# Kernel optimization log

Hardware: AMD Instinct MI355X
Metric: run time of the kernel (lower is better)

Reference implementation:

```python
import jax, jax.numpy as jnp
import numpy as np

N = 100000   # nodes
E = 1600000  # edges
G = 64       # graphs in batch
IN, H, F1, OUT = 3, 64, 256, 10
EPS = 1e-5


def setup_inputs() -> dict:
    key = jax.random.key(0)
    ks = jax.random.split(key, 16)
    d = {}
    d["x"] = jax.random.normal(ks[0], (N, IN), dtype=jnp.float32)
    d["membership"] = jnp.sort(jax.random.randint(ks[1], (N,), 0, G))
    d["edges"] = jax.random.randint(ks[2], (2, E), 0, N)
    def lin(k, fan_in, shape):
        return jax.random.uniform(k, shape, jnp.float32, -1.0, 1.0) / np.sqrt(fan_in)
    # GraphConv1: out = lin_rel(agg) + lin_root(x); lin_root has no bias in PyG
    d["W_rel1"] = lin(ks[3], IN, (IN, H)); d["b_rel1"] = jnp.zeros((H,), jnp.float32)
    d["W_root1"] = lin(ks[4], IN, (IN, H))
    d["W_rel2"] = lin(ks[5], H, (H, H)); d["b_rel2"] = jnp.zeros((H,), jnp.float32)
    d["W_root2"] = lin(ks[6], H, (H, H))
    d["g1"] = jnp.ones((H,), jnp.float32); d["b1"] = jnp.zeros((H,), jnp.float32)
    d["g2"] = jnp.ones((H,), jnp.float32); d["b2"] = jnp.zeros((H,), jnp.float32)
    d["W_fc1"] = lin(ks[7], H, (H, F1)); d["b_fc1"] = lin(ks[8], H, (F1,))
    d["g3"] = jnp.ones((F1,), jnp.float32); d["b3"] = jnp.zeros((F1,), jnp.float32)
    d["W_fc2"] = lin(ks[9], F1, (F1, OUT)); d["b_fc2"] = lin(ks[10], F1, (OUT,))
    return d


def _bn(h, g, b):
    # BatchNorm1d in training mode: biased batch variance
    m = h.mean(axis=0)
    v = h.var(axis=0)
    return (h - m) * jax.lax.rsqrt(v + EPS) * g + b


def reference(x, membership, edges, W_rel1, b_rel1, W_root1, W_rel2, b_rel2,
              W_root2, g1, b1, g2, b2, W_fc1, b_fc1, g3, b3, W_fc2, b_fc2):
    src, dst = edges[0], edges[1]

    def gconv(h, Wr, br, Wroot):
        # message = x_j (edge_weight=None); aggr='add' at target node
        agg = jax.ops.segment_sum(h[src], dst, num_segments=N)
        return agg @ Wr + br + h @ Wroot

    h = _bn(jax.nn.relu(gconv(x, W_rel1, b_rel1, W_root1)), g1, b1)
    h = _bn(jax.nn.relu(gconv(h, W_rel2, b_rel2, W_root2)), g2, b2)
    # global mean pool over graph membership
    cnt = jax.ops.segment_sum(jnp.ones((N,), h.dtype), membership, num_segments=G)
    pooled = jax.ops.segment_sum(h, membership, num_segments=G) / jnp.maximum(cnt, 1.0)[:, None]
    z = _bn(jax.nn.relu(pooled @ W_fc1 + b_fc1), g3, b3)
    return z @ W_fc2 + b_fc2
```

## Files before the change

kernel.cpp:

```cpp
#include <hip/hip_runtime.h>
#include <hip/hip_bf16.h>

#define EPSV 1e-5f
#define BKT 128
#define NB  782

typedef __hip_bfloat16 bf16;
typedef __attribute__((ext_vector_type(8))) short short8v;
typedef __attribute__((ext_vector_type(4))) float f32x4v;

__device__ inline void atomAddG(float* p, float v) { unsafeAtomicAdd(p, v); }
__device__ inline unsigned short f2bf(float v) {
    bf16 h = __float2bfloat16(v);
    return *reinterpret_cast<unsigned short*>(&h);
}

__global__ __launch_bounds__(256) void bhist_kernel(
    const int* __restrict__ edges, int* __restrict__ gbcnt, int E)
{
    __shared__ int lh[NB];
    const int t = threadIdx.x;
    for (int i = t; i < NB; i += 256) lh[i] = 0;
    __syncthreads();
    const int base = blockIdx.x * 4096;
    #pragma unroll
    for (int i = 0; i < 16; ++i) {
        int e = base + i * 256 + t;
        if (e < E) atomicAdd(&lh[edges[E + e] >> 7], 1);
    }
    __syncthreads();
    for (int i = t; i < NB; i += 256) {
        int c = lh[i];
        if (c) atomicAdd(&gbcnt[i], c);
    }
}

__global__ __launch_bounds__(256) void bscan_kernel(
    const int* __restrict__ gbcnt, int* __restrict__ bbase,
    int* __restrict__ gcursor, int E)
{
    __shared__ int l[256];
    const int t = threadIdx.x;
    int b0 = t * 4;
    int v0 = (b0 + 0 < NB) ? gbcnt[b0 + 0] : 0;
    int v1 = (b0 + 1 < NB) ? gbcnt[b0 + 1] : 0;
    int v2 = (b0 + 2 < NB) ? gbcnt[b0 + 2] : 0;
    int v3 = (b0 + 3 < NB) ? gbcnt[b0 + 3] : 0;
    int tot = v0 + v1 + v2 + v3;
    l[t] = tot;
    __syncthreads();
    for (int o = 1; o < 256; o <<= 1) {
        int add = (t >= o) ? l[t - o] : 0;
        __syncthreads();
        l[t] += add;
        __syncthreads();
    }
    int off = l[t] - tot;
    if (b0 + 0 < NB) { bbase[b0 + 0] = off;                gcursor[b0 + 0] = off; }
    if (b0 + 1 < NB) { bbase[b0 + 1] = off + v0;           gcursor[b0 + 1] = off + v0; }
    if (b0 + 2 < NB) { bbase[b0 + 2] = off + v0 + v1;      gcursor[b0 + 2] = off + v0 + v1; }
    if (b0 + 3 < NB) { bbase[b0 + 3] = off + v0 + v1 + v2; gcursor[b0 + 3] = off + v0 + v1 + v2; }
    if (t == 0) bbase[NB] = E;
}

__global__ __launch_bounds__(256) void bfill_kernel(
    const int* __restrict__ edges, int* __restrict__ gcursor,
    int* __restrict__ pk, int E)
{
    __shared__ int lh[NB];
    __shared__ int lbase[NB];
    const int t = threadIdx.x;
    for (int i = t; i < NB; i += 256) lh[i] = 0;
    __syncthreads();
    const int base = blockIdx.x * 4096;
    int dv[16];
    #pragma unroll
    for (int i = 0; i < 16; ++i) {
        int e = base + i * 256 + t;
        dv[i] = (e < E) ? edges[E + e] : -1;
        if (dv[i] >= 0) atomicAdd(&lh[dv[i] >> 7], 1);
    }
    __syncthreads();
    for (int i = t; i < NB; i += 256) {
        int c = lh[i];
        lbase[i] = c ? atomicAdd(&gcursor[i], c) : 0;
        lh[i] = 0;
    }
    __syncthreads();
    #pragma unroll
    for (int i = 0; i < 16; ++i) {
        int e = base + i * 256 + t;
        if (dv[i] >= 0) {
            int s = edges[e];
            int b = dv[i] >> 7;
            int pos = lbase[b] + atomicAdd(&lh[b], 1);
            pk[pos] = (s << 7) | (dv[i] & 127);
        }
    }
}

__global__ __launch_bounds__(256) void bsort_kernel(
    const int* __restrict__ pk, const int* __restrict__ bbase,
    const float* __restrict__ x,
    int* __restrict__ rowstart, int* __restrict__ srcs,
    float* __restrict__ agg1, int N, int E)
{
    __shared__ int lcnt[BKT];
    __shared__ int lscan[BKT];
    __shared__ float accx[BKT * 4];
    const int t = threadIdx.x;
    const int b = blockIdx.x;
    const int e0 = bbase[b], e1 = bbase[b + 1];
    if (t < BKT) lcnt[t] = 0;
    for (int i = t; i < BKT * 4; i += 256) accx[i] = 0.f;
    __syncthreads();
    for (int e = e0 + t; e < e1; e += 256) atomicAdd(&lcnt[pk[e] & 127], 1);
    __syncthreads();
    if (t < BKT) lscan[t] = lcnt[t];
    __syncthreads();
    for (int o = 1; o < BKT; o <<= 1) {
        int add = (t < BKT && t >= o) ? lscan[t - o] : 0;
        __syncthreads();
        if (t < BKT) lscan[t] += add;
        __syncthreads();
    }
    const int n0 = b * BKT;
    if (t < BKT) {
        int excl = lscan[t] - lcnt[t];
        lscan[t] = excl;
        int n = n0 + t;
        if (n <= N) rowstart[n] = e0 + excl;
        lcnt[t] = 0;
    }
    __syncthreads();
    for (int e = e0 + t; e < e1; e += 256) {
        int v = pk[e];
        int ld = v & 127;
        int s = v >> 7;
        int pos = atomicAdd(&lcnt[ld], 1);
        srcs[e0 + lscan[ld] + pos] = s;
        atomicAdd(&accx[ld * 4 + 0], x[s * 3 + 0]);
        atomicAdd(&accx[ld * 4 + 1], x[s * 3 + 1]);
        atomicAdd(&accx[ld * 4 + 2], x[s * 3 + 2]);
    }
    __syncthreads();
    for (int i = t; i < BKT * 3; i += 256) {
        int nl = i / 3, c = i - nl * 3;
        int n = n0 + nl;
        if (n < N) agg1[n * 3 + c] = accx[nl * 4 + c];
    }
}

__global__ __launch_bounds__(256) void bounds_kernel(
    const int* __restrict__ membership, int* __restrict__ gstart, int N)
{
    int n = blockIdx.x * 256 + threadIdx.x;
    if (n > N) return;
    int mp = (n == 0) ? -1 : membership[n - 1];
    int mc = (n == N) ? 64 : membership[n];
    for (int g = mp + 1; g <= mc; ++g) gstart[g] = n;
}

__global__ __launch_bounds__(256) void layer1_kernel(
    const float* __restrict__ x, const float* __restrict__ agg1,
    const float* __restrict__ W_rel1, const float* __restrict__ b_rel1,
    const float* __restrict__ W_root1,
    unsigned short* __restrict__ u1b, float* __restrict__ sums, float* __restrict__ sumsq,
    int N)
{
    const int t = threadIdx.x;
    const int f = t & 63, r4 = t >> 6;
    const float wr0 = W_rel1[f], wr1 = W_rel1[64 + f], wr2 = W_rel1[128 + f];
    const float wo0 = W_root1[f], wo1 = W_root1[64 + f], wo2 = W_root1[128 + f];
    const float bb = b_rel1[f];
    float ps = 0.f, pq = 0.f;
    const int base = blockIdx.x * 128;
    for (int i = r4; i < 128; i += 4) {
        int n = base + i;
        if (n >= N) break;
        float a0 = agg1[n * 3 + 0], a1 = agg1[n * 3 + 1], a2 = agg1[n * 3 + 2];
        float x0 = x[n * 3 + 0], x1 = x[n * 3 + 1], x2 = x[n * 3 + 2];
        float v = bb;
        v = fmaf(a0, wr0, v); v = fmaf(a1, wr1, v); v = fmaf(a2, wr2, v);
        v = fmaf(x0, wo0, v); v = fmaf(x1, wo1, v); v = fmaf(x2, wo2, v);
        v = fmaxf(v, 0.f);
        u1b[n * 64 + f] = f2bf(v);
        ps += v; pq += v * v;
    }
    __shared__ float lsum[4][64], lsq[4][64];
    lsum[r4][f] = ps; lsq[r4][f] = pq;
    __syncthreads();
    if (r4 == 0) {
        float s = lsum[0][f] + lsum[1][f] + lsum[2][f] + lsum[3][f];
        float q = lsq[0][f] + lsq[1][f] + lsq[2][f] + lsq[3][f];
        atomAddG(&sums[f], s);
        atomAddG(&sumsq[f], q);
    }
}

__global__ void bnscale_kernel(const float* __restrict__ sums, const float* __restrict__ sumsq,
                               const float* __restrict__ g, const float* __restrict__ b,
                               float invn, int C,
                               float* __restrict__ scale, float* __restrict__ shift)
{
    int f = blockIdx.x * blockDim.x + threadIdx.x;
    if (f >= C) return;
    float m = sums[f] * invn;
    float v = sumsq[f] * invn - m * m;
    float sc = g[f] * rsqrtf(v + EPSV);
    scale[f] = sc;
    shift[f] = b[f] - m * sc;
}

__global__ __launch_bounds__(256) void bnfold_kernel(
    const float* __restrict__ scale1, const float* __restrict__ shift1,
    const float* __restrict__ W_rel2, const float* __restrict__ W_root2,
    const float* __restrict__ b_rel2,
    unsigned short* __restrict__ wrelp, unsigned short* __restrict__ wrootp,
    float* __restrict__ crel, float* __restrict__ croot)
{
    __shared__ float r1[4][64], r2[4][64];
    const int t = threadIdx.x, f = t & 63, kg = t >> 6;
    float c1 = 0.f, c2 = 0.f;
    for (int k = kg * 16; k < kg * 16 + 16; ++k) {
        float sc = scale1[k], sh = shift1[k];
        float w1 = W_rel2[k * 64 + f], w2 = W_root2[k * 64 + f];
        wrelp[k * 64 + f] = f2bf(sc * w1);
        wrootp[k * 64 + f] = f2bf(sc * w2);
        c1 = fmaf(sh, w1, c1); c2 = fmaf(sh, w2, c2);
    }
    r1[kg][f] = c1; r2[kg][f] = c2;
    __syncthreads();
    if (kg == 0) {
        crel[f]  = r1[0][f] + r1[1][f] + r1[2][f] + r1[3][f];
        croot[f] = r2[0][f] + r2[1][f] + r2[2][f] + r2[3][f] + b_rel2[f];
    }
}

__global__ __launch_bounds__(256) void mfma_transform_kernel(
    const unsigned short* __restrict__ u1b,
    const unsigned short* __restrict__ wrelp, const unsigned short* __restrict__ wrootp,
    const float* __restrict__ crel, const float* __restrict__ croot,
    unsigned short* __restrict__ tb, unsigned short* __restrict__ pb, int NT)
{
    const int wid = (blockIdx.x * blockDim.x + threadIdx.x) >> 6;
    const int lane = threadIdx.x & 63;
    const int q = lane >> 4, r = lane & 15;

    short8v Bf[2][8];
    float cadd[8];
    #pragma unroll
    for (int kc = 0; kc < 2; ++kc) {
        #pragma unroll
        for (int ft = 0; ft < 8; ++ft) {
            const unsigned short* W = (ft < 4) ? wrelp : wrootp;
            const int f0 = (ft & 3) * 16;
            short8v b;
            #pragma unroll
            for (int j = 0; j < 8; ++j) {
                int k = 32 * kc + 8 * q + j;
                b[j] = (short)W[k * 64 + f0 + r];
            }
            Bf[kc][ft] = b;
        }
    }
    #pragma unroll
    for (int ft = 0; ft < 8; ++ft)
        cadd[ft] = (ft < 4) ? crel[(ft & 3) * 16 + r] : croot[(ft & 3) * 16 + r];

    const int totalWaves = (gridDim.x * blockDim.x) >> 6;
    for (int tile = wid; tile < NT; tile += totalWaves) {
        const int n0 = tile * 16;
        short8v A0 = *(const short8v*)&u1b[(n0 + r) * 64 + 8 * q];
        short8v A1 = *(const short8v*)&u1b[(n0 + r) * 64 + 32 + 8 * q];
        #pragma unroll
        for (int ft = 0; ft < 8; ++ft) {
            f32x4v d = {0.f, 0.f, 0.f, 0.f};
            d = __builtin_amdgcn_mfma_f32_16x16x32_bf16(A0, Bf[0][ft], d, 0, 0, 0);
            d = __builtin_amdgcn_mfma_f32_16x16x32_bf16(A1, Bf[1][ft], d, 0, 0, 0);
            unsigned short* O = (ft < 4) ? tb : pb;
            const int f0 = (ft & 3) * 16;
            const float ca = cadd[ft];
            #pragma unroll
            for (int rr = 0; rr < 4; ++rr) {
                int n = n0 + 4 * q + rr;
                O[n * 64 + f0 + r] = f2bf(d[rr] + ca);
            }
        }
    }
}

__global__ __launch_bounds__(256, 8) void gatherpool_kernel(
    const bf16* __restrict__ tb, const bf16* __restrict__ pb,
    const int* __restrict__ rowstart, const int* __restrict__ srcs,
    const int* __restrict__ membership,
    float* __restrict__ pooled, float* __restrict__ sums, float* __restrict__ sumsq,
    int N, int chunk)
{
    __shared__ float red[4][64];
    const int tid = threadIdx.x;
    const int w = tid >> 6, f = tid & 63;
    const int gw = __builtin_amdgcn_readfirstlane(blockIdx.x * 4 + w);
    const int n0 = gw * chunk;
    const int n1 = min(N, n0 + chunk);
    float ps = 0.f, pq = 0.f, pacc = 0.f;
    int curg = (n0 < N) ? membership[n0] : -1;

    for (int n = n0; n < n1; ++n) {
        int s0 = rowstart[n], s1 = rowstart[n + 1];
        float acc = __bfloat162float(pb[n * 64 + f]);
        int j = s0;
        for (; j + 15 < s1; j += 16) {
            float vs[16];
            #pragma unroll
            for (int q = 0; q < 16; ++q)
                vs[q] = __bfloat162float(tb[srcs[j + q] * 64 + f]);
            float sA = ((vs[0] + vs[1]) + (vs[2] + vs[3])) + ((vs[4] + vs[5]) + (vs[6] + vs[7]));
            float sB = ((vs[8] + vs[9]) + (vs[10] + vs[11])) + ((vs[12] + vs[13]) + (vs[14] + vs[15]));
            acc += sA + sB;
        }
        for (; j + 3 < s1; j += 4) {
            float v0 = __bfloat162float(tb[srcs[j + 0] * 64 + f]);
            float v1 = __bfloat162float(tb[srcs[j + 1] * 64 + f]);
            float v2 = __bfloat162float(tb[srcs[j + 2] * 64 + f]);
            float v3 = __bfloat162float(tb[srcs[j + 3] * 64 + f]);
            acc += (v0 + v1) + (v2 + v3);
        }
        for (; j < s1; ++j) acc += __bfloat162float(tb[srcs[j] * 64 + f]);

        acc = fmaxf(acc, 0.f);
        ps += acc; pq += acc * acc;

        int g = membership[n];
        if (g != curg) {
            atomAddG(&pooled[curg * 64 + f], pacc);
            pacc = 0.f;
            curg = g;
        }
        pacc += acc;
    }
    if (curg >= 0) atomAddG(&pooled[curg * 64 + f], pacc);

    red[w][f] = ps;
    __syncthreads();
    if (w == 0) atomAddG(&sums[f], red[0][f] + red[1][f] + red[2][f] + red[3][f]);
    __syncthreads();
    red[w][f] = pq;
    __syncthreads();
    if (w == 0) atomAddG(&sumsq[f], red[0][f] + red[1][f] + red[2][f] + red[3][f]);
}

__global__ __launch_bounds__(1024) void fc1_kernel(
    const float* __restrict__ pooled, const int* __restrict__ gstart,
    const float* __restrict__ scale2, const float* __restrict__ shift2,
    const float* __restrict__ W_fc1, const float* __restrict__ b_fc1,
    const float* __restrict__ g3, const float* __restrict__ b3,
    float* __restrict__ z)
{
    __shared__ float pm[4096];
    __shared__ float reds[4][256], redq[4][256];
    __shared__ float lsc[256], lsh[256];
    const int t = threadIdx.x;
    for (int i = t; i < 4096; i += 1024) {
        int g = i >> 6, f = i & 63;
        float c = fmaxf((float)(gstart[g + 1] - gstart[g]), 1.0f);
        pm[i] = fmaf(pooled[i] / c, scale2[f], shift2[f]);
    }
    __syncthreads();
    const int col = t & 255, grp = t >> 8;
    float acc[16];
    const float bc = b_fc1[col];
    #pragma unroll
    for (int g = 0; g < 16; ++g) acc[g] = bc;
    for (int k = 0; k < 64; ++k) {
        float wv = W_fc1[k * 256 + col];
        #pragma unroll
        for (int g = 0; g < 16; ++g)
            acc[g] = fmaf(pm[(grp * 16 + g) * 64 + k], wv, acc[g]);
    }
    float s = 0.f, q = 0.f;
    #pragma unroll
    for (int g = 0; g < 16; ++g) {
        acc[g] = fmaxf(acc[g], 0.f);
        s += acc[g]; q += acc[g] * acc[g];
    }
    reds[grp][col] = s; redq[grp][col] = q;
    __syncthreads();
    if (grp == 0) {
        float S = reds[0][col] + reds[1][col] + reds[2][col] + reds[3][col];
        float Q = redq[0][col] + redq[1][col] + redq[2][col] + redq[3][col];
        float m = S * (1.0f / 64.0f);
        float v = Q * (1.0f / 64.0f) - m * m;
        float sc = g3[col] * rsqrtf(v + EPSV);
        lsc[col] = sc;
        lsh[col] = b3[col] - m * sc;
    }
    __syncthreads();
    float sc = lsc[col], sh = lsh[col];
    #pragma unroll
    for (int g = 0; g < 16; ++g)
        z[(grp * 16 + g) * 256 + col] = fmaf(acc[g], sc, sh);
}

__global__ __launch_bounds__(640) void fc2_kernel(
    const float* __restrict__ z, const float* __restrict__ W_fc2,
    const float* __restrict__ b_fc2, float* __restrict__ out)
{
    int t = threadIdx.x;
    int g = t / 10, o = t % 10;
    float acc = b_fc2[o];
    for (int c = 0; c < 256; ++c)
        acc = fmaf(z[g * 256 + c], W_fc2[c * 10 + o], acc);
    out[g * 10 + o] = acc;
}

extern "C" void kernel_launch(void* const* d_in, const int* in_sizes, int n_in,
                              void* d_out, int out_size, void* d_ws, size_t ws_size,
                              hipStream_t stream) {
    const int N = 100000, E = 1600000;

    const float* x          = (const float*)d_in[0];
    const int*   membership = (const int*)d_in[1];
    const int*   edges      = (const int*)d_in[2];
    const float* W_rel1     = (const float*)d_in[3];
    const float* b_rel1     = (const float*)d_in[4];
    const float* W_root1    = (const float*)d_in[5];
    const float* W_rel2     = (const float*)d_in[6];
    const float* b_rel2     = (const float*)d_in[7];
    const float* W_root2    = (const float*)d_in[8];
    const float* g1         = (const float*)d_in[9];
    const float* b1         = (const float*)d_in[10];
    const float* g2         = (const float*)d_in[11];
    const float* b2         = (const float*)d_in[12];
    const float* W_fc1      = (const float*)d_in[13];
    const float* b_fc1      = (const float*)d_in[14];
    const float* g3         = (const float*)d_in[15];
    const float* b3         = (const float*)d_in[16];
    const float* W_fc2      = (const float*)d_in[17];
    const float* b_fc2      = (const float*)d_in[18];

    int*   wsi      = (int*)d_ws;
    float* wsf      = (float*)d_ws;
    int*   gbcnt    = wsi + 0;
    float* stats    = wsf + 784;
    float* pooled   = wsf + 1296;
    int*   bbase    = wsi + 5392;
    int*   gcursor  = wsi + 6192;
    int*   gstart   = wsi + 6976;
    int*   rowstart = wsi + 7104;
    int*   pk       = wsi + 107168;
    int*   srcs     = wsi + 1707168;
    float* agg1     = wsf + 3307168;
    unsigned short* u1b = (unsigned short*)(wsf + 3607200);
    unsigned short* tb  = (unsigned short*)(wsf + 6807200);
    unsigned short* pb  = (unsigned short*)(wsf + 10007200);
    unsigned short* wrelp  = (unsigned short*)(wsf + 13207200);
    unsigned short* wrootp = (unsigned short*)(wsf + 13209248);
    float* crel     = wsf + 13211296;
    float* croot    = wsf + 13211360;
    float* z        = wsf + 13211424;

    float* sums1  = stats + 0;
    float* sumsq1 = stats + 64;
    float* sums2  = stats + 128;
    float* sumsq2 = stats + 192;
    float* scale1 = stats + 256;
    float* shift1 = stats + 320;
    float* scale2 = stats + 384;
    float* shift2 = stats + 448;

    hipMemsetAsync(d_ws, 0, (size_t)(784 + 512 + 4096) * 4, stream);

    const int EB = (E + 4095) / 4096;
    bhist_kernel<<<EB, 256, 0, stream>>>(edges, gbcnt, E);
    bscan_kernel<<<1, 256, 0, stream>>>(gbcnt, bbase, gcursor, E);
    bfill_kernel<<<EB, 256, 0, stream>>>(edges, gcursor, pk, E);
    bsort_kernel<<<NB, 256, 0, stream>>>(pk, bbase, x, rowstart, srcs, agg1, N, E);
    bounds_kernel<<<(N + 256) / 256, 256, 0, stream>>>(membership, gstart, N);

    layer1_kernel<<<(N + 127) / 128, 256, 0, stream>>>(
        x, agg1, W_rel1, b_rel1, W_root1, u1b, sums1, sumsq1, N);
    bnscale_kernel<<<1, 64, 0, stream>>>(sums1, sumsq1, g1, b1, 1.0f / N, 64, scale1, shift1);

    bnfold_kernel<<<1, 256, 0, stream>>>(scale1, shift1, W_rel2, W_root2, b_rel2,
                                         wrelp, wrootp, crel, croot);
    mfma_transform_kernel<<<512, 256, 0, stream>>>(
        u1b, wrelp, wrootp, crel, croot, tb, pb, N / 16);

    {
        const int GRID2 = 2048;
        int chunk = (N + GRID2 * 4 - 1) / (GRID2 * 4);
        gatherpool_kernel<<<GRID2, 256, 0, stream>>>(
            (const bf16*)tb, (const bf16*)pb, rowstart, srcs, membership,
            pooled, sums2, sumsq2, N, chunk);
    }
    bnscale_kernel<<<1, 64, 0, stream>>>(sums2, sumsq2, g2, b2, 1.0f / N, 64, scale2, shift2);

    fc1_kernel<<<1, 1024, 0, stream>>>(pooled, gstart, scale2, shift2,
                                       W_fc1, b_fc1, g3, b3, z);
    fc2_kernel<<<1, 640, 0, stream>>>(z, W_fc2, b_fc2, (float*)d_out);
}
```

Before: 254.3 us.

## Use 1024-node sort buckets, interleave two-row gathers, fuse BN-scale and fc kernels

The counting sort now uses 98 buckets of 1024 destinations instead of 782 buckets of 128, and the per-bucket sort runs with 1024-thread blocks. The gather-pool loop processes two destination rows at once with 8-wide unrolls, so more independent loads are in flight. The layer-1 BN scale computation is folded into bnfold, and fc2 is merged into fc1, which removes two launches. The trade-off is that the bucket sort kernel gets only 98 blocks, which gives low parallelism on a large GPU.

```diff
diff --git a/kernel.cpp b/kernel.cpp
--- a/kernel.cpp
+++ b/kernel.cpp
@@ -2,8 +2,8 @@
 #include <hip/hip_bf16.h>
 
 #define EPSV 1e-5f
-#define BKT 128
-#define NB  782
+#define CB   1024
+#define NBC  98
 
 typedef __hip_bfloat16 bf16;
 typedef __attribute__((ext_vector_type(8))) short short8v;
@@ -14,63 +14,61 @@
     bf16 h = __float2bfloat16(v);
     return *reinterpret_cast<unsigned short*>(&h);
 }
+__device__ inline float bfu(unsigned short u) {
+    return __uint_as_float(((unsigned int)u) << 16);
+}
 
 __global__ __launch_bounds__(256) void bhist_kernel(
     const int* __restrict__ edges, int* __restrict__ gbcnt, int E)
 {
-    __shared__ int lh[NB];
+    __shared__ int lh[NBC];
     const int t = threadIdx.x;
-    for (int i = t; i < NB; i += 256) lh[i] = 0;
+    if (t < NBC) lh[t] = 0;
     __syncthreads();
     const int base = blockIdx.x * 4096;
     #pragma unroll
     for (int i = 0; i < 16; ++i) {
         int e = base + i * 256 + t;
-        if (e < E) atomicAdd(&lh[edges[E + e] >> 7], 1);
-    }
-    __syncthreads();
-    for (int i = t; i < NB; i += 256) {
-        int c = lh[i];
-        if (c) atomicAdd(&gbcnt[i], c);
-    }
-}
-
-__global__ __launch_bounds__(256) void bscan_kernel(
+        if (e < E) atomicAdd(&lh[edges[E + e] >> 10], 1);
+    }
+    __syncthreads();
+    if (t < NBC) {
+        int c = lh[t];
+        if (c) atomicAdd(&gbcnt[t], c);
+    }
+}
+
+__global__ __launch_bounds__(128) void bscan_kernel(
     const int* __restrict__ gbcnt, int* __restrict__ bbase,
     int* __restrict__ gcursor, int E)
 {
-    __shared__ int l[256];
+    __shared__ int l[128];
     const int t = threadIdx.x;
-    int b0 = t * 4;
-    int v0 = (b0 + 0 < NB) ? gbcnt[b0 + 0] : 0;
-    int v1 = (b0 + 1 < NB) ? gbcnt[b0 + 1] : 0;
-    int v2 = (b0 + 2 < NB) ? gbcnt[b0 + 2] : 0;
-    int v3 = (b0 + 3 < NB) ? gbcnt[b0 + 3] : 0;
-    int tot = v0 + v1 + v2 + v3;
-    l[t] = tot;
-    __syncthreads();
-    for (int o = 1; o < 256; o <<= 1) {
+    int v = (t < NBC) ? gbcnt[t] : 0;
+    l[t] = v;
+    __syncthreads();
+    for (int o = 1; o < 128; o <<= 1) {
         int add = (t >= o) ? l[t - o] : 0;
         __syncthreads();
         l[t] += add;
         __syncthreads();
     }
-    int off = l[t] - tot;
-    if (b0 + 0 < NB) { bbase[b0 + 0] = off;                gcursor[b0 + 0] = off; }
-    if (b0 + 1 < NB) { bbase[b0 + 1] = off + v0;           gcursor[b0 + 1] = off + v0; }
-    if (b0 + 2 < NB) { bbase[b0 + 2] = off + v0 + v1;      gcursor[b0 + 2] = off + v0 + v1; }
-    if (b0 + 3 < NB) { bbase[b0 + 3] = off + v0 + v1 + v2; gcursor[b0 + 3] = off + v0 + v1 + v2; }
-    if (t == 0) bbase[NB] = E;
+    if (t < NBC) {
+        int off = l[t] - v;
+        bbase[t] = off;
+        gcursor[t] = off;
+    }
+    if (t == 0) bbase[NBC] = E;
 }
 
 __global__ __launch_bounds__(256) void bfill_kernel(
     const int* __restrict__ edges, int* __restrict__ gcursor,
     int* __restrict__ pk, int E)
 {
-    __shared__ int lh[NB];
-    __shared__ int lbase[NB];
+    __shared__ int lh[NBC];
+    __shared__ int lbase[NBC];
     const int t = threadIdx.x;
-    for (int i = t; i < NB; i += 256) lh[i] = 0;
+    if (t < NBC) lh[t] = 0;
     __syncthreads();
     const int base = blockIdx.x * 4096;
     int dv[16];
@@ -78,13 +76,13 @@
     for (int i = 0; i < 16; ++i) {
         int e = base + i * 256 + t;
         dv[i] = (e < E) ? edges[E + e] : -1;
-        if (dv[i] >= 0) atomicAdd(&lh[dv[i] >> 7], 1);
-    }
-    __syncthreads();
-    for (int i = t; i < NB; i += 256) {
-        int c = lh[i];
-        lbase[i] = c ? atomicAdd(&gcursor[i], c) : 0;
-        lh[i] = 0;
+        if (dv[i] >= 0) atomicAdd(&lh[dv[i] >> 10], 1);
+    }
+    __syncthreads();
+    if (t < NBC) {
+        int c = lh[t];
+        lbase[t] = c ? atomicAdd(&gcursor[t], c) : 0;
+        lh[t] = 0;
     }
     __syncthreads();
     #pragma unroll
@@ -92,51 +90,50 @@
         int e = base + i * 256 + t;
         if (dv[i] >= 0) {
             int s = edges[e];
-            int b = dv[i] >> 7;
+            int b = dv[i] >> 10;
             int pos = lbase[b] + atomicAdd(&lh[b], 1);
-            pk[pos] = (s << 7) | (dv[i] & 127);
-        }
-    }
-}
-
-__global__ __launch_bounds__(256) void bsort_kernel(
+            pk[pos] = (s << 10) | (dv[i] & 1023);
+        }
+    }
+}
+
+__global__ __launch_bounds__(1024) void bsortB_kernel(
     const int* __restrict__ pk, const int* __restrict__ bbase,
     const float* __restrict__ x,
     int* __restrict__ rowstart, int* __restrict__ srcs,
     float* __restrict__ agg1, int N, int E)
 {
-    __shared__ int lcnt[BKT];
-    __shared__ int lscan[BKT];
-    __shared__ float accx[BKT * 4];
+    __shared__ int lcnt[CB];
+    __shared__ int lscan[CB];
+    __shared__ float accx[CB * 4];
     const int t = threadIdx.x;
     const int b = blockIdx.x;
     const int e0 = bbase[b], e1 = bbase[b + 1];
-    if (t < BKT) lcnt[t] = 0;
-    for (int i = t; i < BKT * 4; i += 256) accx[i] = 0.f;
-    __syncthreads();
-    for (int e = e0 + t; e < e1; e += 256) atomicAdd(&lcnt[pk[e] & 127], 1);
-    __syncthreads();
-    if (t < BKT) lscan[t] = lcnt[t];
-    __syncthreads();
-    for (int o = 1; o < BKT; o <<= 1) {
-        int add = (t < BKT && t >= o) ? lscan[t - o] : 0;
+    lcnt[t] = 0;
+    #pragma unroll
+    for (int i = 0; i < 4; ++i) accx[i * CB + t] = 0.f;
+    __syncthreads();
+    for (int e = e0 + t; e < e1; e += 1024) atomicAdd(&lcnt[pk[e] & 1023], 1);
+    __syncthreads();
+    lscan[t] = lcnt[t];
+    __syncthreads();
+    for (int o = 1; o < CB; o <<= 1) {
+        int add = (t >= o) ? lscan[t - o] : 0;
         __syncthreads();
-        if (t < BKT) lscan[t] += add;
+        lscan[t] += add;
         __syncthreads();
     }
-    const int n0 = b * BKT;
-    if (t < BKT) {
-        int excl = lscan[t] - lcnt[t];
-        lscan[t] = excl;
-        int n = n0 + t;
-        if (n <= N) rowstart[n] = e0 + excl;
-        lcnt[t] = 0;
-    }
-    __syncthreads();
-    for (int e = e0 + t; e < e1; e += 256) {
+    const int n0 = b * CB;
+    int excl = lscan[t] - lcnt[t];
+    int n = n0 + t;
+    if (n <= N) rowstart[n] = e0 + excl;
+    lscan[t] = excl;
+    lcnt[t] = 0;
+    __syncthreads();
+    for (int e = e0 + t; e < e1; e += 1024) {
         int v = pk[e];
-        int ld = v & 127;
-        int s = v >> 7;
+        int ld = v & 1023;
+        int s = v >> 10;
         int pos = atomicAdd(&lcnt[ld], 1);
         srcs[e0 + lscan[ld] + pos] = s;
         atomicAdd(&accx[ld * 4 + 0], x[s * 3 + 0]);
@@ -144,10 +141,10 @@
         atomicAdd(&accx[ld * 4 + 2], x[s * 3 + 2]);
     }
     __syncthreads();
-    for (int i = t; i < BKT * 3; i += 256) {
+    for (int i = t; i < CB * 3; i += 1024) {
         int nl = i / 3, c = i - nl * 3;
-        int n = n0 + nl;
-        if (n < N) agg1[n * 3 + c] = accx[nl * 4 + c];
+        int nn = n0 + nl;
+        if (nn < N) agg1[nn * 3 + c] = accx[nl * 4 + c];
     }
 }
 
@@ -213,17 +210,27 @@
 }
 
 __global__ __launch_bounds__(256) void bnfold_kernel(
-    const float* __restrict__ scale1, const float* __restrict__ shift1,
+    const float* __restrict__ sums1, const float* __restrict__ sumsq1,
+    const float* __restrict__ g1, const float* __restrict__ b1,
     const float* __restrict__ W_rel2, const float* __restrict__ W_root2,
     const float* __restrict__ b_rel2,
     unsigned short* __restrict__ wrelp, unsigned short* __restrict__ wrootp,
-    float* __restrict__ crel, float* __restrict__ croot)
-{
+    float* __restrict__ crel, float* __restrict__ croot, float invn)
+{
+    __shared__ float lsc[64], lsh[64];
     __shared__ float r1[4][64], r2[4][64];
     const int t = threadIdx.x, f = t & 63, kg = t >> 6;
+    if (t < 64) {
+        float m = sums1[t] * invn;
+        float v = sumsq1[t] * invn - m * m;
+        float sc = g1[t] * rsqrtf(v + EPSV);
+        lsc[t] = sc;
+        lsh[t] = b1[t] - m * sc;
+    }
+    __syncthreads();
     float c1 = 0.f, c2 = 0.f;
     for (int k = kg * 16; k < kg * 16 + 16; ++k) {
-        float sc = scale1[k], sh = shift1[k];
+        float sc = lsc[k], sh = lsh[k];
         float w1 = W_rel2[k * 64 + f], w2 = W_root2[k * 64 + f];
         wrelp[k * 64 + f] = f2bf(sc * w1);
         wrootp[k * 64 + f] = f2bf(sc * w2);
@@ -255,13 +262,13 @@
         for (int ft = 0; ft < 8; ++ft) {
             const unsigned short* W = (ft < 4) ? wrelp : wrootp;
             const int f0 = (ft & 3) * 16;
-            short8v b;
+            short8v bb;
             #pragma unroll
             for (int j = 0; j < 8; ++j) {
                 int k = 32 * kc + 8 * q + j;
-                b[j] = (short)W[k * 64 + f0 + r];
+                bb[j] = (short)W[k * 64 + f0 + r];
             }
-            Bf[kc][ft] = b;
+            Bf[kc][ft] = bb;
         }
     }
     #pragma unroll
@@ -291,7 +298,7 @@
 }
 
 __global__ __launch_bounds__(256, 8) void gatherpool_kernel(
-    const bf16* __restrict__ tb, const bf16* __restrict__ pb,
+    const unsigned short* __restrict__ tb, const unsigned short* __restrict__ pb,
     const int* __restrict__ rowstart, const int* __restrict__ srcs,
     const int* __restrict__ membership,
     float* __restrict__ pooled, float* __restrict__ sums, float* __restrict__ sumsq,
@@ -306,38 +313,60 @@
     float ps = 0.f, pq = 0.f, pacc = 0.f;
     int curg = (n0 < N) ? membership[n0] : -1;
 
-    for (int n = n0; n < n1; ++n) {
-        int s0 = rowstart[n], s1 = rowstart[n + 1];
-        float acc = __bfloat162float(pb[n * 64 + f]);
-        int j = s0;
-        for (; j + 15 < s1; j += 16) {
-            float vs[16];
+    for (int n = n0; n < n1; n += 2) {
+        const bool two = (n + 1 < n1);
+        int sA0 = rowstart[n], sA1 = rowstart[n + 1];
+        int sB1 = two ? rowstart[n + 2] : sA1;
+        int degA = sA1 - sA0, degB = sB1 - sA1;
+        float accA = bfu(pb[n * 64 + f]);
+        float accB = two ? bfu(pb[(n + 1) * 64 + f]) : 0.f;
+
+        int mA = degA & ~7, mB = degB & ~7;
+        int m = min(mA, mB);
+        int k = 0;
+        for (; k < m; k += 8) {
+            float va[8], vb[8];
             #pragma unroll
-            for (int q = 0; q < 16; ++q)
-                vs[q] = __bfloat162float(tb[srcs[j + q] * 64 + f]);
-            float sA = ((vs[0] + vs[1]) + (vs[2] + vs[3])) + ((vs[4] + vs[5]) + (vs[6] + vs[7]));
-            float sB = ((vs[8] + vs[9]) + (vs[10] + vs[11])) + ((vs[12] + vs[13]) + (vs[14] + vs[15]));
-            acc += sA + sB;
-        }
-        for (; j + 3 < s1; j += 4) {
-            float v0 = __bfloat162float(tb[srcs[j + 0] * 64 + f]);
-            float v1 = __bfloat162float(tb[srcs[j + 1] * 64 + f]);
-            float v2 = __bfloat162float(tb[srcs[j + 2] * 64 + f]);
-            float v3 = __bfloat162float(tb[srcs[j + 3] * 64 + f]);
-            acc += (v0 + v1) + (v2 + v3);
-        }
-        for (; j < s1; ++j) acc += __bfloat162float(tb[srcs[j] * 64 + f]);
-
-        acc = fmaxf(acc, 0.f);
-        ps += acc; pq += acc * acc;
-
-        int g = membership[n];
-        if (g != curg) {
+            for (int u = 0; u < 8; ++u) va[u] = bfu(tb[srcs[sA0 + k + u] * 64 + f]);
+            #pragma unroll
+            for (int u = 0; u < 8; ++u) vb[u] = bfu(tb[srcs[sA1 + k + u] * 64 + f]);
+            accA += ((va[0] + va[1]) + (va[2] + va[3])) + ((va[4] + va[5]) + (va[6] + va[7]));
+            accB += ((vb[0] + vb[1]) + (vb[2] + vb[3])) + ((vb[4] + vb[5]) + (vb[6] + vb[7]));
+        }
+        for (int ka = k; ka < mA; ka += 8) {
+            float va[8];
+            #pragma unroll
+            for (int u = 0; u < 8; ++u) va[u] = bfu(tb[srcs[sA0 + ka + u] * 64 + f]);
+            accA += ((va[0] + va[1]) + (va[2] + va[3])) + ((va[4] + va[5]) + (va[6] + va[7]));
+        }
+        for (int kb = k; kb < mB; kb += 8) {
+            float vb[8];
+            #pragma unroll
+            for (int u = 0; u < 8; ++u) vb[u] = bfu(tb[srcs[sA1 + kb + u] * 64 + f]);
+            accB += ((vb[0] + vb[1]) + (vb[2] + vb[3])) + ((vb[4] + vb[5]) + (vb[6] + vb[7]));
+        }
+        for (int ka = mA; ka < degA; ++ka) accA += bfu(tb[srcs[sA0 + ka] * 64 + f]);
+        for (int kb = mB; kb < degB; ++kb) accB += bfu(tb[srcs[sA1 + kb] * 64 + f]);
+
+        accA = fmaxf(accA, 0.f);
+        ps += accA; pq += accA * accA;
+        int gA = membership[n];
+        if (gA != curg) {
             atomAddG(&pooled[curg * 64 + f], pacc);
-            pacc = 0.f;
-            curg = g;
-        }
-        pacc += acc;
+            pacc = 0.f; curg = gA;
+        }
+        pacc += accA;
+
+        if (two) {
+            accB = fmaxf(accB, 0.f);
+            ps += accB; pq += accB * accB;
+            int gB = membership[n + 1];
+            if (gB != curg) {
+                atomAddG(&pooled[curg * 64 + f], pacc);
+                pacc = 0.f; curg = gB;
+            }
+            pacc += accB;
+        }
     }
     if (curg >= 0) atomAddG(&pooled[curg * 64 + f], pacc);
 
@@ -350,12 +379,13 @@
     if (w == 0) atomAddG(&sumsq[f], red[0][f] + red[1][f] + red[2][f] + red[3][f]);
 }
 
-__global__ __launch_bounds__(1024) void fc1_kernel(
+__global__ __launch_bounds__(1024) void fc12_kernel(
     const float* __restrict__ pooled, const int* __restrict__ gstart,
     const float* __restrict__ scale2, const float* __restrict__ shift2,
     const float* __restrict__ W_fc1, const float* __restrict__ b_fc1,
     const float* __restrict__ g3, const float* __restrict__ b3,
-    float* __restrict__ z)
+    const float* __restrict__ W_fc2, const float* __restrict__ b_fc2,
+    float* __restrict__ z, float* __restrict__ out)
 {
     __shared__ float pm[4096];
     __shared__ float reds[4][256], redq[4][256];
@@ -400,18 +430,14 @@
     #pragma unroll
     for (int g = 0; g < 16; ++g)
         z[(grp * 16 + g) * 256 + col] = fmaf(acc[g], sc, sh);
-}
-
-__global__ __launch_bounds__(640) void fc2_kernel(
-    const float* __restrict__ z, const float* __restrict__ W_fc2,
-    const float* __restrict__ b_fc2, float* __restrict__ out)
-{
-    int t = threadIdx.x;
-    int g = t / 10, o = t % 10;
-    float acc = b_fc2[o];
-    for (int c = 0; c < 256; ++c)
-        acc = fmaf(z[g * 256 + c], W_fc2[c * 10 + o], acc);
-    out[g * 10 + o] = acc;
+    __syncthreads();
+    if (t < 640) {
+        int g = t / 10, o = t % 10;
+        float a = b_fc2[o];
+        for (int c = 0; c < 256; ++c)
+            a = fmaf(z[g * 256 + c], W_fc2[c * 10 + o], a);
+        out[g * 10 + o] = a;
+    }
 }
 
 extern "C" void kernel_launch(void* const* d_in, const int* in_sizes, int n_in,
@@ -464,8 +490,6 @@
     float* sumsq1 = stats + 64;
     float* sums2  = stats + 128;
     float* sumsq2 = stats + 192;
-    float* scale1 = stats + 256;
-    float* shift1 = stats + 320;
     float* scale2 = stats + 384;
     float* shift2 = stats + 448;
 
@@ -473,17 +497,17 @@
 
     const int EB = (E + 4095) / 4096;
     bhist_kernel<<<EB, 256, 0, stream>>>(edges, gbcnt, E);
-    bscan_kernel<<<1, 256, 0, stream>>>(gbcnt, bbase, gcursor, E);
+    bscan_kernel<<<1, 128, 0, stream>>>(gbcnt, bbase, gcursor, E);
     bfill_kernel<<<EB, 256, 0, stream>>>(edges, gcursor, pk, E);
-    bsort_kernel<<<NB, 256, 0, stream>>>(pk, bbase, x, rowstart, srcs, agg1, N, E);
+    bsortB_kernel<<<NBC, 1024, 0, stream>>>(pk, bbase, x, rowstart, srcs, agg1, N, E);
     bounds_kernel<<<(N + 256) / 256, 256, 0, stream>>>(membership, gstart, N);
 
     layer1_kernel<<<(N + 127) / 128, 256, 0, stream>>>(
         x, agg1, W_rel1, b_rel1, W_root1, u1b, sums1, sumsq1, N);
-    bnscale_kernel<<<1, 64, 0, stream>>>(sums1, sumsq1, g1, b1, 1.0f / N, 64, scale1, shift1);
-
-    bnfold_kernel<<<1, 256, 0, stream>>>(scale1, shift1, W_rel2, W_root2, b_rel2,
-                                         wrelp, wrootp, crel, croot);
+
+    bnfold_kernel<<<1, 256, 0, stream>>>(sums1, sumsq1, g1, b1,
+                                         W_rel2, W_root2, b_rel2,
+                                         wrelp, wrootp, crel, croot, 1.0f / N);
     mfma_transform_kernel<<<512, 256, 0, stream>>>(
         u1b, wrelp, wrootp, crel, croot, tb, pb, N / 16);
 
@@ -491,12 +515,11 @@
         const int GRID2 = 2048;
         int chunk = (N + GRID2 * 4 - 1) / (GRID2 * 4);
         gatherpool_kernel<<<GRID2, 256, 0, stream>>>(
-            (const bf16*)tb, (const bf16*)pb, rowstart, srcs, membership,
-            pooled, sums2, sumsq2, N, chunk);
+            tb, pb, rowstart, srcs, membership, pooled, sums2, sumsq2, N, chunk);
     }
     bnscale_kernel<<<1, 64, 0, stream>>>(sums2, sumsq2, g2, b2, 1.0f / N, 64, scale2, shift2);
 
-    fc1_kernel<<<1, 1024, 0, stream>>>(pooled, gstart, scale2, shift2,
-                                       W_fc1, b_fc1, g3, b3, z);
-    fc2_kernel<<<1, 640, 0, stream>>>(z, W_fc2, b_fc2, (float*)d_out);
-}
+    fc12_kernel<<<1, 1024, 0, stream>>>(pooled, gstart, scale2, shift2,
+                                        W_fc1, b_fc1, g3, b3, W_fc2, b_fc2,
+                                        z, (float*)d_out);
+}
```

Result: slower. 276.3 us (+8.6%).

## Fuse BN scale kernels, stage bucket keys in LDS, dynamic gather scheduling

Applied to the files above, without the earlier changes.

Folds the BatchNorm scale/shift computation into the consumer kernels and fuses fc1 with fc2, removing three small launches. bsort caches each bucket's packed keys in shared memory to avoid re-reading them, and reads a float4-padded copy of x produced by a new pad kernel. gatherpool replaces static per-wave node ranges with an atomic work cursor handing out 5-node chunks, plus an extra 8-wide tail step. This adds one launch, more pooled atomics per chunk, and cursor contention.

```diff
diff --git a/kernel.cpp b/kernel.cpp
--- a/kernel.cpp
+++ b/kernel.cpp
@@ -4,6 +4,8 @@
 #define EPSV 1e-5f
 #define BKT 128
 #define NB  782
+#define LPK 4096
+#define GCHUNK 5
 
 typedef __hip_bfloat16 bf16;
 typedef __attribute__((ext_vector_type(8))) short short8v;
@@ -13,6 +15,9 @@
 __device__ inline unsigned short f2bf(float v) {
     bf16 h = __float2bfloat16(v);
     return *reinterpret_cast<unsigned short*>(&h);
+}
+__device__ inline float bfu(unsigned short u) {
+    return __uint_as_float(((unsigned int)u) << 16);
 }
 
 __global__ __launch_bounds__(256) void bhist_kernel(
@@ -99,22 +104,38 @@
     }
 }
 
+__global__ __launch_bounds__(256) void xpad_kernel(
+    const float* __restrict__ x, float* __restrict__ xp, int N)
+{
+    int n = blockIdx.x * 256 + threadIdx.x;
+    if (n >= N) return;
+    float4 v;
+    v.x = x[n * 3 + 0]; v.y = x[n * 3 + 1]; v.z = x[n * 3 + 2]; v.w = 0.f;
+    *(float4*)&xp[n * 4] = v;
+}
+
 __global__ __launch_bounds__(256) void bsort_kernel(
     const int* __restrict__ pk, const int* __restrict__ bbase,
-    const float* __restrict__ x,
+    const float* __restrict__ xp,
     int* __restrict__ rowstart, int* __restrict__ srcs,
     float* __restrict__ agg1, int N, int E)
 {
     __shared__ int lcnt[BKT];
     __shared__ int lscan[BKT];
     __shared__ float accx[BKT * 4];
+    __shared__ int lpk[LPK];
     const int t = threadIdx.x;
     const int b = blockIdx.x;
     const int e0 = bbase[b], e1 = bbase[b + 1];
+    const int cnt = e1 - e0;
     if (t < BKT) lcnt[t] = 0;
     for (int i = t; i < BKT * 4; i += 256) accx[i] = 0.f;
-    __syncthreads();
-    for (int e = e0 + t; e < e1; e += 256) atomicAdd(&lcnt[pk[e] & 127], 1);
+    for (int i = t; i < cnt && i < LPK; i += 256) lpk[i] = pk[e0 + i];
+    __syncthreads();
+    for (int i = t; i < cnt; i += 256) {
+        int v = (i < LPK) ? lpk[i] : pk[e0 + i];
+        atomicAdd(&lcnt[v & 127], 1);
+    }
     __syncthreads();
     if (t < BKT) lscan[t] = lcnt[t];
     __syncthreads();
@@ -133,15 +154,16 @@
         lcnt[t] = 0;
     }
     __syncthreads();
-    for (int e = e0 + t; e < e1; e += 256) {
-        int v = pk[e];
+    for (int i = t; i < cnt; i += 256) {
+        int v = (i < LPK) ? lpk[i] : pk[e0 + i];
         int ld = v & 127;
         int s = v >> 7;
         int pos = atomicAdd(&lcnt[ld], 1);
         srcs[e0 + lscan[ld] + pos] = s;
-        atomicAdd(&accx[ld * 4 + 0], x[s * 3 + 0]);
-        atomicAdd(&accx[ld * 4 + 1], x[s * 3 + 1]);
-        atomicAdd(&accx[ld * 4 + 2], x[s * 3 + 2]);
+        float4 xv = *(const float4*)&xp[s * 4];
+        atomicAdd(&accx[ld * 4 + 0], xv.x);
+        atomicAdd(&accx[ld * 4 + 1], xv.y);
+        atomicAdd(&accx[ld * 4 + 2], xv.z);
     }
     __syncthreads();
     for (int i = t; i < BKT * 3; i += 256) {
@@ -198,32 +220,28 @@
     }
 }
 
-__global__ void bnscale_kernel(const float* __restrict__ sums, const float* __restrict__ sumsq,
-                               const float* __restrict__ g, const float* __restrict__ b,
-                               float invn, int C,
-                               float* __restrict__ scale, float* __restrict__ shift)
-{
-    int f = blockIdx.x * blockDim.x + threadIdx.x;
-    if (f >= C) return;
-    float m = sums[f] * invn;
-    float v = sumsq[f] * invn - m * m;
-    float sc = g[f] * rsqrtf(v + EPSV);
-    scale[f] = sc;
-    shift[f] = b[f] - m * sc;
-}
-
 __global__ __launch_bounds__(256) void bnfold_kernel(
-    const float* __restrict__ scale1, const float* __restrict__ shift1,
+    const float* __restrict__ sums1, const float* __restrict__ sumsq1,
+    const float* __restrict__ g1, const float* __restrict__ b1,
     const float* __restrict__ W_rel2, const float* __restrict__ W_root2,
     const float* __restrict__ b_rel2,
     unsigned short* __restrict__ wrelp, unsigned short* __restrict__ wrootp,
-    float* __restrict__ crel, float* __restrict__ croot)
-{
+    float* __restrict__ crel, float* __restrict__ croot, float invn)
+{
+    __shared__ float lsc[64], lsh[64];
     __shared__ float r1[4][64], r2[4][64];
     const int t = threadIdx.x, f = t & 63, kg = t >> 6;
+    if (t < 64) {
+        float m = sums1[t] * invn;
+        float v = sumsq1[t] * invn - m * m;
+        float sc = g1[t] * rsqrtf(v + EPSV);
+        lsc[t] = sc;
+        lsh[t] = b1[t] - m * sc;
+    }
+    __syncthreads();
     float c1 = 0.f, c2 = 0.f;
     for (int k = kg * 16; k < kg * 16 + 16; ++k) {
-        float sc = scale1[k], sh = shift1[k];
+        float sc = lsc[k], sh = lsh[k];
         float w1 = W_rel2[k * 64 + f], w2 = W_root2[k * 64 + f];
         wrelp[k * 64 + f] = f2bf(sc * w1);
         wrootp[k * 64 + f] = f2bf(sc * w2);
@@ -255,13 +273,13 @@
         for (int ft = 0; ft < 8; ++ft) {
             const unsigned short* W = (ft < 4) ? wrelp : wrootp;
             const int f0 = (ft & 3) * 16;
-            short8v b;
+            short8v bb;
             #pragma unroll
             for (int j = 0; j < 8; ++j) {
                 int k = 32 * kc + 8 * q + j;
-                b[j] = (short)W[k * 64 + f0 + r];
+                bb[j] = (short)W[k * 64 + f0 + r];
             }
-            Bf[kc][ft] = b;
+            Bf[kc][ft] = bb;
         }
     }
     #pragma unroll
@@ -291,55 +309,72 @@
 }
 
 __global__ __launch_bounds__(256, 8) void gatherpool_kernel(
-    const bf16* __restrict__ tb, const bf16* __restrict__ pb,
+    const unsigned short* __restrict__ tb, const unsigned short* __restrict__ pb,
     const int* __restrict__ rowstart, const int* __restrict__ srcs,
     const int* __restrict__ membership,
+    int* __restrict__ cursor,
     float* __restrict__ pooled, float* __restrict__ sums, float* __restrict__ sumsq,
-    int N, int chunk)
+    int N)
 {
     __shared__ float red[4][64];
     const int tid = threadIdx.x;
     const int w = tid >> 6, f = tid & 63;
-    const int gw = __builtin_amdgcn_readfirstlane(blockIdx.x * 4 + w);
-    const int n0 = gw * chunk;
-    const int n1 = min(N, n0 + chunk);
-    float ps = 0.f, pq = 0.f, pacc = 0.f;
-    int curg = (n0 < N) ? membership[n0] : -1;
-
-    for (int n = n0; n < n1; ++n) {
-        int s0 = rowstart[n], s1 = rowstart[n + 1];
-        float acc = __bfloat162float(pb[n * 64 + f]);
-        int j = s0;
-        for (; j + 15 < s1; j += 16) {
-            float vs[16];
-            #pragma unroll
-            for (int q = 0; q < 16; ++q)
-                vs[q] = __bfloat162float(tb[srcs[j + q] * 64 + f]);
-            float sA = ((vs[0] + vs[1]) + (vs[2] + vs[3])) + ((vs[4] + vs[5]) + (vs[6] + vs[7]));
-            float sB = ((vs[8] + vs[9]) + (vs[10] + vs[11])) + ((vs[12] + vs[13]) + (vs[14] + vs[15]));
-            acc += sA + sB;
+    float ps = 0.f, pq = 0.f;
+
+    for (;;) {
+        int c = 0;
+        if (f == 0) c = atomicAdd(cursor, 1);
+        c = __shfl(c, 0, 64);
+        int n0 = c * GCHUNK;
+        if (n0 >= N) break;
+        int n1 = min(N, n0 + GCHUNK);
+        float pacc = 0.f;
+        int curg = membership[n0];
+
+        for (int n = n0; n < n1; ++n) {
+            int s0 = rowstart[n], s1 = rowstart[n + 1];
+            float acc = bfu(pb[n * 64 + f]);
+            int j = s0;
+            for (; j + 15 < s1; j += 16) {
+                float vs[16];
+                #pragma unroll
+                for (int q = 0; q < 16; ++q)
+                    vs[q] = bfu(tb[srcs[j + q] * 64 + f]);
+                float sA = ((vs[0] + vs[1]) + (vs[2] + vs[3])) + ((vs[4] + vs[5]) + (vs[6] + vs[7]));
+                float sB = ((vs[8] + vs[9]) + (vs[10] + vs[11])) + ((vs[12] + vs[13]) + (vs[14] + vs[15]));
+                acc += sA + sB;
+            }
+            if (j + 7 < s1) {
+                float vs[8];
+                #pragma unroll
+                for (int q = 0; q < 8; ++q)
+                    vs[q] = bfu(tb[srcs[j + q] * 64 + f]);
+                acc += ((vs[0] + vs[1]) + (vs[2] + vs[3])) + ((vs[4] + vs[5]) + (vs[6] + vs[7]));
+                j += 8;
+            }
+            if (j + 3 < s1) {
+                float v0 = bfu(tb[srcs[j + 0] * 64 + f]);
+                float v1 = bfu(tb[srcs[j + 1] * 64 + f]);
+                float v2 = bfu(tb[srcs[j + 2] * 64 + f]);
+                float v3 = bfu(tb[srcs[j + 3] * 64 + f]);
+                acc += (v0 + v1) + (v2 + v3);
+                j += 4;
+            }
+            for (; j < s1; ++j) acc += bfu(tb[srcs[j] * 64 + f]);
+
+            acc = fmaxf(acc, 0.f);
+            ps += acc; pq += acc * acc;
+
+            int g = membership[n];
+            if (g != curg) {
+                atomAddG(&pooled[curg * 64 + f], pacc);
+                pacc = 0.f;
+                curg = g;
+            }
+            pacc += acc;
         }
-        for (; j + 3 < s1; j += 4) {
-            float v0 = __bfloat162float(tb[srcs[j + 0] * 64 + f]);
-            float v1 = __bfloat162float(tb[srcs[j + 1] * 64 + f]);
-            float v2 = __bfloat162float(tb[srcs[j + 2] * 64 + f]);
-            float v3 = __bfloat162float(tb[srcs[j + 3] * 64 + f]);
-            acc += (v0 + v1) + (v2 + v3);
-        }
-        for (; j < s1; ++j) acc += __bfloat162float(tb[srcs[j] * 64 + f]);
-
-        acc = fmaxf(acc, 0.f);
-        ps += acc; pq += acc * acc;
-
-        int g = membership[n];
-        if (g != curg) {
-            atomAddG(&pooled[curg * 64 + f], pacc);
-            pacc = 0.f;
-            curg = g;
-        }
-        pacc += acc;
-    }
-    if (curg >= 0) atomAddG(&pooled[curg * 64 + f], pacc);
+        atomAddG(&pooled[curg * 64 + f], pacc);
+    }
 
     red[w][f] = ps;
     __syncthreads();
@@ -350,21 +385,32 @@
     if (w == 0) atomAddG(&sumsq[f], red[0][f] + red[1][f] + red[2][f] + red[3][f]);
 }
 
-__global__ __launch_bounds__(1024) void fc1_kernel(
+__global__ __launch_bounds__(1024) void fc12_kernel(
     const float* __restrict__ pooled, const int* __restrict__ gstart,
-    const float* __restrict__ scale2, const float* __restrict__ shift2,
+    const float* __restrict__ sums2, const float* __restrict__ sumsq2,
+    const float* __restrict__ g2, const float* __restrict__ b2, float invn,
     const float* __restrict__ W_fc1, const float* __restrict__ b_fc1,
     const float* __restrict__ g3, const float* __restrict__ b3,
-    float* __restrict__ z)
+    const float* __restrict__ W_fc2, const float* __restrict__ b_fc2,
+    float* __restrict__ z, float* __restrict__ out)
 {
     __shared__ float pm[4096];
     __shared__ float reds[4][256], redq[4][256];
     __shared__ float lsc[256], lsh[256];
+    __shared__ float sc2[64], sh2[64];
     const int t = threadIdx.x;
+    if (t < 64) {
+        float m = sums2[t] * invn;
+        float v = sumsq2[t] * invn - m * m;
+        float sc = g2[t] * rsqrtf(v + EPSV);
+        sc2[t] = sc;
+        sh2[t] = b2[t] - m * sc;
+    }
+    __syncthreads();
     for (int i = t; i < 4096; i += 1024) {
         int g = i >> 6, f = i & 63;
         float c = fmaxf((float)(gstart[g + 1] - gstart[g]), 1.0f);
-        pm[i] = fmaf(pooled[i] / c, scale2[f], shift2[f]);
+        pm[i] = fmaf(pooled[i] / c, sc2[f], sh2[f]);
     }
     __syncthreads();
     const int col = t & 255, grp = t >> 8;
@@ -400,18 +446,14 @@
     #pragma unroll
     for (int g = 0; g < 16; ++g)
         z[(grp * 16 + g) * 256 + col] = fmaf(acc[g], sc, sh);
-}
-
-__global__ __launch_bounds__(640) void fc2_kernel(
-    const float* __restrict__ z, const float* __restrict__ W_fc2,
-    const float* __restrict__ b_fc2, float* __restrict__ out)
-{
-    int t = threadIdx.x;
-    int g = t / 10, o = t % 10;
-    float acc = b_fc2[o];
-    for (int c = 0; c < 256; ++c)
-        acc = fmaf(z[g * 256 + c], W_fc2[c * 10 + o], acc);
-    out[g * 10 + o] = acc;
+    __syncthreads();
+    if (t < 640) {
+        int g = t / 10, o = t % 10;
+        float a = b_fc2[o];
+        for (int c = 0; c < 256; ++c)
+            a = fmaf(z[g * 256 + c], W_fc2[c * 10 + o], a);
+        out[g * 10 + o] = a;
+    }
 }
 
 extern "C" void kernel_launch(void* const* d_in, const int* in_sizes, int n_in,
@@ -459,44 +501,37 @@
     float* crel     = wsf + 13211296;
     float* croot    = wsf + 13211360;
     float* z        = wsf + 13211424;
+    float* xp       = wsf + 13227808;
 
     float* sums1  = stats + 0;
     float* sumsq1 = stats + 64;
     float* sums2  = stats + 128;
     float* sumsq2 = stats + 192;
-    float* scale1 = stats + 256;
-    float* shift1 = stats + 320;
-    float* scale2 = stats + 384;
-    float* shift2 = stats + 448;
+    int*   curs   = wsi + 783;
 
     hipMemsetAsync(d_ws, 0, (size_t)(784 + 512 + 4096) * 4, stream);
 
     const int EB = (E + 4095) / 4096;
+    xpad_kernel<<<(N + 255) / 256, 256, 0, stream>>>(x, xp, N);
     bhist_kernel<<<EB, 256, 0, stream>>>(edges, gbcnt, E);
     bscan_kernel<<<1, 256, 0, stream>>>(gbcnt, bbase, gcursor, E);
     bfill_kernel<<<EB, 256, 0, stream>>>(edges, gcursor, pk, E);
-    bsort_kernel<<<NB, 256, 0, stream>>>(pk, bbase, x, rowstart, srcs, agg1, N, E);
+    bsort_kernel<<<NB, 256, 0, stream>>>(pk, bbase, xp, rowstart, srcs, agg1, N, E);
     bounds_kernel<<<(N + 256) / 256, 256, 0, stream>>>(membership, gstart, N);
 
     layer1_kernel<<<(N + 127) / 128, 256, 0, stream>>>(
         x, agg1, W_rel1, b_rel1, W_root1, u1b, sums1, sumsq1, N);
-    bnscale_kernel<<<1, 64, 0, stream>>>(sums1, sumsq1, g1, b1, 1.0f / N, 64, scale1, shift1);
-
-    bnfold_kernel<<<1, 256, 0, stream>>>(scale1, shift1, W_rel2, W_root2, b_rel2,
-                                         wrelp, wrootp, crel, croot);
+
+    bnfold_kernel<<<1, 256, 0, stream>>>(sums1, sumsq1, g1, b1,
+                                         W_rel2, W_root2, b_rel2,
+                                         wrelp, wrootp, crel, croot, 1.0f / N);
     mfma_transform_kernel<<<512, 256, 0, stream>>>(
         u1b, wrelp, wrootp, crel, croot, tb, pb, N / 16);
 
-    {
-        const int GRID2 = 2048;
-        int chunk = (N + GRID2 * 4 - 1) / (GRID2 * 4);
-        gatherpool_kernel<<<GRID2, 256, 0, stream>>>(
-            (const bf16*)tb, (const bf16*)pb, rowstart, srcs, membership,
-            pooled, sums2, sumsq2, N, chunk);
-    }
-    bnscale_kernel<<<1, 64, 0, stream>>>(sums2, sumsq2, g2, b2, 1.0f / N, 64, scale2, shift2);
-
-    fc1_kernel<<<1, 1024, 0, stream>>>(pooled, gstart, scale2, shift2,
-                                       W_fc1, b_fc1, g3, b3, z);
-    fc2_kernel<<<1, 640, 0, stream>>>(z, W_fc2, b_fc2, (float*)d_out);
-}
+    gatherpool_kernel<<<2048, 256, 0, stream>>>(
+        tb, pb, rowstart, srcs, membership, curs, pooled, sums2, sumsq2, N);
+
+    fc12_kernel<<<1, 1024, 0, stream>>>(pooled, gstart, sums2, sumsq2, g2, b2, 1.0f / N,
+                                        W_fc1, b_fc1, g3, b3, W_fc2, b_fc2,
+                                        z, (float*)d_out);
+}
```

New measurement: 514.3 us. 2.02x slower.
